# Performance work log

Hardware: AMD Instinct MI355X
Metric: run time of the kernel (lower is better)

The kernel has to match this reference:

```python
import jax, jax.numpy as jnp
import numpy as np

EPS = 1e-6
TEMPERATURE = 0.75
SINKHORN_ITERS = 7
BUCKETS = 128


def setup_inputs() -> dict:
    key = jax.random.key(0)
    k1, k2, k3, k4, k5 = jax.random.split(key, 5)
    b, h, t, dh = 2, 8, 8192, 128
    q = jax.random.normal(k1, (b, h, t, dh), dtype=jnp.float32)
    k = jax.random.normal(k2, (b, h, t, dh), dtype=jnp.float32)
    v = jax.random.normal(k3, (b, h, t, dh), dtype=jnp.float32)
    # SimpleSortNet linear: (1, heads, 2*dim_head, buckets)
    W_sort = jax.random.normal(k4, (1, h, 2 * dh, BUCKETS), dtype=jnp.float32)
    # uniform noise used to build gumbel samples (torch samples internally)
    u_gumbel = jax.random.uniform(k5, (b * h, BUCKETS, BUCKETS), dtype=jnp.float32)
    return {"q": q, "k": k, "v": v, "W_sort": W_sort, "u_gumbel": u_gumbel}


def _gumbel_sinkhorn(R, u):
    # R >= 0 (post-relu). r = (log(R+eps) + gumbel) / temperature
    g = -jnp.log(-jnp.log(u + EPS) + EPS)
    r = (jnp.log(R + EPS) + g) / TEMPERATURE
    for _ in range(SINKHORN_ITERS):
        r = r - jax.nn.logsumexp(r, axis=2, keepdims=True)
        r = r - jax.nn.logsumexp(r, axis=1, keepdims=True)
    return jnp.exp(r)


def reference(q, k, v, W_sort, u_gumbel):
    b, h, t, dh = q.shape
    dim = h * dh  # full model dim, used for the softmax scale (matches torch)
    bh = b * h
    buckets = W_sort.shape[-1]
    bsz = t // buckets

    qm = q.reshape(bh, t, dh)
    km = k.reshape(bh, t, dh)
    vm = v.reshape(bh, t, dh)

    b_q = qm.reshape(bh, buckets, bsz, dh)
    b_k = km.reshape(bh, buckets, bsz, dh)
    b_v = vm.reshape(bh, buckets, bsz, dh)

    # SimpleSortNet: per-bucket sums of q and k -> linear -> relu
    x = jnp.concatenate([b_q.sum(axis=2), b_k.sum(axis=2)], axis=-1)  # (bh, buckets, 2*dh)
    W = jnp.broadcast_to(W_sort, (b, h, 2 * dh, buckets)).reshape(bh, 2 * dh, buckets)
    R = jax.nn.relu(jnp.einsum('bue,bek->buk', x, W))  # (bh, buckets, buckets)

    R = _gumbel_sinkhorn(R, u_gumbel)

    # zero_all_but_top along dim=2 with k=1 (keep argmax entry per row)
    idx = jnp.argmax(R, axis=2, keepdims=True)  # (bh, buckets, 1)
    mask = jnp.arange(buckets)[None, None, :] == idx
    R = jnp.where(mask, R, 0.0)

    # reorder buckets: butd = sum_v R[buv] * b_k[bvtd]
    b_k_r = jnp.einsum('buv,bvtd->butd', R, b_k)
    b_v_r = jnp.einsum('buv,bvtd->butd', R, b_v)

    b_k_cat = jnp.concatenate([b_k_r, b_k], axis=2)  # (bh, buckets, 2*bsz, dh)
    b_v_cat = jnp.concatenate([b_v_r, b_v], axis=2)

    dots = jnp.einsum('buie,buje->buij', b_q, b_k_cat) * (dim ** -0.5)
    attn = jax.nn.softmax(dots, axis=-1)
    out = jnp.einsum('buij,buje->buie', attn, b_v_cat)  # (bh, buckets, bsz, dh)

    return out.reshape(b, h, t, dh)
```

## Files before the change

kernel.cpp:

```cpp
#include <hip/hip_runtime.h>
#include <hip/hip_bf16.h>

#define T_SEQ   8192
#define DH      128
#define NBH     16
#define NBUCK   128
#define BSZ     64
#define EPSF    1e-6f

#define SWZ(r) (((((r) & 7) ^ (((r) >> 3) & 7))) << 3)

typedef __attribute__((ext_vector_type(8))) __bf16 bf16x8;
typedef __attribute__((ext_vector_type(4))) float  f32x4;

static __device__ __forceinline__ unsigned short f2bf(float f) {
  __bf16 h = (__bf16)f;
  return __builtin_bit_cast(unsigned short, h);
}

__global__ __launch_bounds__(256) void k_bsum(
    const float* __restrict__ q, const float* __restrict__ k,
    float* __restrict__ x) {
  const int u = blockIdx.x, bh = blockIdx.y, which = blockIdx.z;
  const int t = threadIdx.x;
  const int c4g = t & 31;
  const int r0  = (t >> 5) << 3;
  const float* src = which ? k : q;
  const float* p = src + ((size_t)bh * T_SEQ + (size_t)u * BSZ + r0) * DH + c4g * 4;
  float4 acc = {0.f, 0.f, 0.f, 0.f};
  #pragma unroll
  for (int r = 0; r < 8; r++) {
    float4 vv = *(const float4*)(p + (size_t)r * DH);
    acc.x += vv.x; acc.y += vv.y; acc.z += vv.z; acc.w += vv.w;
  }
  __shared__ float4 xr[8][32];
  xr[t >> 5][c4g] = acc;
  __syncthreads();
  if (t < 32) {
    float4 s4 = xr[0][t];
    #pragma unroll
    for (int j = 1; j < 8; j++) {
      float4 o = xr[j][t];
      s4.x += o.x; s4.y += o.y; s4.z += o.z; s4.w += o.w;
    }
    *(float4*)(x + ((size_t)bh * NBUCK + u) * 256 + which * 128 + t * 4) = s4;
  }
}

__global__ __launch_bounds__(128) void k_sortgemm(
    const float* __restrict__ x, const float* __restrict__ W,
    const float* __restrict__ ug, float* __restrict__ rbuf) {
  const int u0 = blockIdx.x * 4, bh = blockIdx.y;
  const int v = threadIdx.x;
  __shared__ float xs[4][256];
  for (int i = v; i < 1024; i += 128)
    xs[i >> 8][i & 255] = x[((size_t)bh * NBUCK + u0 + (i >> 8)) * 256 + (i & 255)];
  __syncthreads();
  const float* Wp = W + (size_t)(bh & 7) * 256 * NBUCK + v;
  float acc0 = 0.f, acc1 = 0.f, acc2 = 0.f, acc3 = 0.f;
  #pragma unroll 16
  for (int e = 0; e < 256; e++) {
    float we = Wp[(size_t)e * NBUCK];
    acc0 += xs[0][e] * we;
    acc1 += xs[1][e] * we;
    acc2 += xs[2][e] * we;
    acc3 += xs[3][e] * we;
  }
  float accs[4] = {acc0, acc1, acc2, acc3};
  #pragma unroll
  for (int j = 0; j < 4; j++) {
    float R = fmaxf(accs[j], 0.f) + EPSF;
    float gu = ug[((size_t)bh * NBUCK + u0 + j) * NBUCK + v] + EPSF;
    float g = -logf(-logf(gu) + EPSF);
    rbuf[((size_t)bh * NBUCK + u0 + j) * NBUCK + v] = (logf(R) + g) * (1.f / 0.75f);
  }
}

__global__ __launch_bounds__(1024) void k_sinkhorn(
    const float* __restrict__ rbuf, int* __restrict__ idxb, float* __restrict__ sb) {
  const int bh = blockIdx.x;
  const int t  = threadIdx.x;
  const int g  = t >> 3;
  const int s  = t & 7;
  __shared__ float rl[128 * 129];
  __shared__ float ca[128], ra[128];

  const float* rb = rbuf + (size_t)bh * (NBUCK * NBUCK);
  for (int i = t; i < NBUCK * NBUCK; i += 1024)
    rl[(i >> 7) * 129 + (i & 127)] = rb[i];
  if (t < 128) ca[t] = 0.f;
  __syncthreads();

  for (int iter = 0; iter < 7; iter++) {
    {
      float vals[16];
      float m = -1e30f;
      #pragma unroll
      for (int i = 0; i < 16; i++) {
        int vv = s * 16 + i;
        vals[i] = rl[g * 129 + vv] + ca[vv];
        m = fmaxf(m, vals[i]);
      }
      m = fmaxf(m, __shfl_xor(m, 1));
      m = fmaxf(m, __shfl_xor(m, 2));
      m = fmaxf(m, __shfl_xor(m, 4));
      float ss = 0.f;
      #pragma unroll
      for (int i = 0; i < 16; i++) ss += __expf(vals[i] - m);
      ss += __shfl_xor(ss, 1);
      ss += __shfl_xor(ss, 2);
      ss += __shfl_xor(ss, 4);
      if (s == 0) ra[g] = -(m + logf(ss));
    }
    __syncthreads();
    {
      float vals[16];
      float m = -1e30f;
      #pragma unroll
      for (int i = 0; i < 16; i++) {
        int uu = s * 16 + i;
        vals[i] = rl[uu * 129 + g] + ra[uu];
        m = fmaxf(m, vals[i]);
      }
      m = fmaxf(m, __shfl_xor(m, 1));
      m = fmaxf(m, __shfl_xor(m, 2));
      m = fmaxf(m, __shfl_xor(m, 4));
      float ss = 0.f;
      #pragma unroll
      for (int i = 0; i < 16; i++) ss += __expf(vals[i] - m);
      ss += __shfl_xor(ss, 1);
      ss += __shfl_xor(ss, 2);
      ss += __shfl_xor(ss, 4);
      if (s == 0) ca[g] = -(m + logf(ss));
    }
    __syncthreads();
  }

  {
    float best = -1e30f; int bi = 0;
    #pragma unroll
    for (int i = 0; i < 16; i++) {
      int vv = s * 16 + i;
      float val = rl[g * 129 + vv] + ca[vv];
      if (val > best) { best = val; bi = vv; }
    }
    #pragma unroll
    for (int d = 1; d < 8; d <<= 1) {
      float ob = __shfl_xor(best, d);
      int   oi = __shfl_xor(bi, d);
      if (ob > best || (ob == best && oi < bi)) { best = ob; bi = oi; }
    }
    if (s == 0) {
      idxb[bh * NBUCK + g] = bi;
      sb[bh * NBUCK + g]   = expf(rl[g * 129 + bi] + ra[g] + ca[bi]);
    }
  }
}

__global__ __launch_bounds__(256) void k_attn(
    const float* __restrict__ q, const float* __restrict__ k, const float* __restrict__ v,
    const int* __restrict__ idxb, const float* __restrict__ sb, float* __restrict__ out) {
  const int u  = blockIdx.x;
  const int bh = blockIdx.y;
  const int t  = threadIdx.x;
  const int lane = t & 63;
  const int w  = t >> 6;
  const int l15 = lane & 15;
  const int lgp = lane >> 4;

  __shared__ uint4 smem4[2048];
  unsigned short* sm = (unsigned short*)smem4;
  #define VOFF 8192

  const int   vidx = idxb[bh * NBUCK + u];
  const float sval = sb[bh * NBUCK + u];
  const size_t hb = (size_t)bh * (T_SEQ * DH);
  const float* qg = q + hb;
  const float* kg = k + hb;
  const float* vg = v + hb;

  #pragma unroll
  for (int it = 0; it < 16; it++) {
    int i = it * 256 + t;
    int row = i >> 5;
    int c4 = (i & 31) << 2;
    int grow = (row < 64) ? (vidx * BSZ + row) : (u * BSZ + (row - 64));
    float4 val = *(const float4*)(kg + (size_t)grow * DH + c4);
    ushort4 hh;
    hh.x = f2bf(val.x); hh.y = f2bf(val.y); hh.z = f2bf(val.z); hh.w = f2bf(val.w);
    *(ushort4*)(sm + (((row * 128 + c4) ^ SWZ(row)))) = hh;
  }

  bf16x8 aQ[4];
  {
    int qrow = u * BSZ + w * 16 + l15;
    const float* qp = qg + (size_t)qrow * DH + lgp * 8;
    #pragma unroll
    for (int kk = 0; kk < 4; kk++) {
      float4 v0 = *(const float4*)(qp + kk * 32);
      float4 v1 = *(const float4*)(qp + kk * 32 + 4);
      bf16x8 f;
      f[0] = (__bf16)v0.x; f[1] = (__bf16)v0.y; f[2] = (__bf16)v0.z; f[3] = (__bf16)v0.w;
      f[4] = (__bf16)v1.x; f[5] = (__bf16)v1.y; f[6] = (__bf16)v1.z; f[7] = (__bf16)v1.w;
      aQ[kk] = f;
    }
  }

  float4 vpre1[8], vpre2[8];
  #pragma unroll
  for (int it = 0; it < 8; it++) {
    int i = it * 256 + t;
    int d0 = (i & 31) << 2;
    int j  = i >> 5;
    vpre1[it] = *(const float4*)(vg + (size_t)(vidx * BSZ + j) * DH + d0);
    vpre2[it] = *(const float4*)(vg + (size_t)(u    * BSZ + j) * DH + d0);
  }
  __syncthreads();

  f32x4 accS[8];
  #pragma unroll
  for (int n = 0; n < 8; n++) {
    f32x4 acc = {0.f, 0.f, 0.f, 0.f};
    #pragma unroll
    for (int kk = 0; kk < 4; kk++) {
      int row = n * 16 + l15;
      int c0 = lgp * 8 + kk * 32;
      bf16x8 bK = *(const bf16x8*)(sm + ((row * 128 + c0) ^ SWZ(row)));
      acc = __builtin_amdgcn_mfma_f32_16x16x32_bf16(aQ[kk], bK, acc, 0, 0, 0);
    }
    accS[n] = acc;
  }

  float pval[8][4];
  float lsum[4];
  #pragma unroll
  for (int r = 0; r < 4; r++) {
    float mm = -1e30f;
    #pragma unroll
    for (int n = 0; n < 8; n++) {
      float lg2 = accS[n][r] * 0.03125f * (n < 4 ? sval : 1.0f);
      pval[n][r] = lg2;
      mm = fmaxf(mm, lg2);
    }
    mm = fmaxf(mm, __shfl_xor(mm, 1));
    mm = fmaxf(mm, __shfl_xor(mm, 2));
    mm = fmaxf(mm, __shfl_xor(mm, 4));
    mm = fmaxf(mm, __shfl_xor(mm, 8));
    float ss = 0.f;
    #pragma unroll
    for (int n = 0; n < 8; n++) {
      float p = __expf(pval[n][r] - mm);
      ss += p;
      pval[n][r] = p * (n < 4 ? sval : 1.0f);
    }
    ss += __shfl_xor(ss, 1);
    ss += __shfl_xor(ss, 2);
    ss += __shfl_xor(ss, 4);
    ss += __shfl_xor(ss, 8);
    lsum[r] = ss;
  }

  __syncthreads();

  #pragma unroll
  for (int n = 0; n < 8; n++) {
    #pragma unroll
    for (int r = 0; r < 4; r++) {
      int prow = w * 16 + lgp * 4 + r;
      int pcol = n * 16 + l15;
      sm[(prow * 128 + pcol) ^ SWZ(prow)] = f2bf(pval[n][r]);
    }
  }
  #pragma unroll
  for (int it = 0; it < 8; it++) {
    int i = it * 256 + t;
    int d0 = (i & 31) << 2;
    int j  = i >> 5;
    float4 val = vpre1[it];
    sm[VOFF + (((d0 + 0) * 64 + j) ^ SWZ(d0 + 0))] = f2bf(val.x);
    sm[VOFF + (((d0 + 1) * 64 + j) ^ SWZ(d0 + 1))] = f2bf(val.y);
    sm[VOFF + (((d0 + 2) * 64 + j) ^ SWZ(d0 + 2))] = f2bf(val.z);
    sm[VOFF + (((d0 + 3) * 64 + j) ^ SWZ(d0 + 3))] = f2bf(val.w);
  }
  __syncthreads();

  bf16x8 aP[4];
  #pragma unroll
  for (int kk = 0; kk < 4; kk++) {
    int prow = w * 16 + l15;
    int c0 = lgp * 8 + kk * 32;
    aP[kk] = *(const bf16x8*)(sm + ((prow * 128 + c0) ^ SWZ(prow)));
  }

  f32x4 accO[8];
  #pragma unroll
  for (int n = 0; n < 8; n++) {
    f32x4 acc = {0.f, 0.f, 0.f, 0.f};
    #pragma unroll
    for (int kk = 0; kk < 2; kk++) {
      int d = n * 16 + l15;
      int jj0 = lgp * 8 + kk * 32;
      bf16x8 bV = *(const bf16x8*)(sm + VOFF + ((d * 64 + jj0) ^ SWZ(d)));
      acc = __builtin_amdgcn_mfma_f32_16x16x32_bf16(aP[kk], bV, acc, 0, 0, 0);
    }
    accO[n] = acc;
  }
  __syncthreads();

  #pragma unroll
  for (int it = 0; it < 8; it++) {
    int i = it * 256 + t;
    int d0 = (i & 31) << 2;
    int j  = i >> 5;
    float4 val = vpre2[it];
    sm[VOFF + (((d0 + 0) * 64 + j) ^ SWZ(d0 + 0))] = f2bf(val.x);
    sm[VOFF + (((d0 + 1) * 64 + j) ^ SWZ(d0 + 1))] = f2bf(val.y);
    sm[VOFF + (((d0 + 2) * 64 + j) ^ SWZ(d0 + 2))] = f2bf(val.z);
    sm[VOFF + (((d0 + 3) * 64 + j) ^ SWZ(d0 + 3))] = f2bf(val.w);
  }
  __syncthreads();

  float invl[4];
  #pragma unroll
  for (int r = 0; r < 4; r++) invl[r] = 1.0f / lsum[r];

  #pragma unroll
  for (int n = 0; n < 8; n++) {
    f32x4 acc = accO[n];
    #pragma unroll
    for (int kk = 2; kk < 4; kk++) {
      int d = n * 16 + l15;
      int jj0 = lgp * 8 + (kk - 2) * 32;
      bf16x8 bV = *(const bf16x8*)(sm + VOFF + ((d * 64 + jj0) ^ SWZ(d)));
      acc = __builtin_amdgcn_mfma_f32_16x16x32_bf16(aP[kk], bV, acc, 0, 0, 0);
    }
    #pragma unroll
    for (int r = 0; r < 4; r++) {
      int i2 = w * 16 + lgp * 4 + r;
      int d = n * 16 + l15;
      out[((size_t)bh * T_SEQ + (size_t)u * BSZ + i2) * DH + d] = acc[r] * invl[r];
    }
  }
}

extern "C" void kernel_launch(void* const* d_in, const int* in_sizes, int n_in,
                              void* d_out, int out_size, void* d_ws, size_t ws_size,
                              hipStream_t stream) {
  (void)in_sizes; (void)n_in; (void)out_size; (void)ws_size;
  const float* q  = (const float*)d_in[0];
  const float* k  = (const float*)d_in[1];
  const float* v  = (const float*)d_in[2];
  const float* W  = (const float*)d_in[3];
  const float* ug = (const float*)d_in[4];
  float* out = (float*)d_out;

  float* xbuf = (float*)d_ws;
  float* rbuf = xbuf + (size_t)NBH * NBUCK * 256;
  int*   idxb = (int*)(rbuf + (size_t)NBH * NBUCK * NBUCK);
  float* sb   = (float*)(idxb + NBH * NBUCK);

  k_bsum    <<<dim3(NBUCK, NBH, 2), 256, 0, stream>>>(q, k, xbuf);
  k_sortgemm<<<dim3(32, NBH),       128, 0, stream>>>(xbuf, W, ug, rbuf);
  k_sinkhorn<<<NBH,                1024, 0, stream>>>(rbuf, idxb, sb);
  k_attn    <<<dim3(NBUCK, NBH),    256, 0, stream>>>(q, k, v, idxb, sb, out);
}
```

Measured before the change: 121.1 us.

## Cache Sinkhorn rows/cols in registers and reorder attention loads with setprio

The Sinkhorn kernel now runs with 512 threads, four per row, and keeps each thread's row and column slice in registers. This removes the repeated shared-memory reads in every iteration, and the exp sums are split across four partial accumulators. The attention kernel issues all K and Q global loads before converting them, and delays the second V prefetch until after the first V tile is written, to lower register pressure. It also adds launch bounds for occupancy and raises wave priority around the MFMA loops. The risks are register spills from the larger per-thread arrays and less latency hiding for the late V load.

```diff
diff --git a/kernel.cpp b/kernel.cpp
--- a/kernel.cpp
+++ b/kernel.cpp
@@ -76,88 +76,113 @@
   }
 }
 
-__global__ __launch_bounds__(1024) void k_sinkhorn(
+__global__ __launch_bounds__(512, 1) void k_sinkhorn(
     const float* __restrict__ rbuf, int* __restrict__ idxb, float* __restrict__ sb) {
   const int bh = blockIdx.x;
   const int t  = threadIdx.x;
-  const int g  = t >> 3;
-  const int s  = t & 7;
+  const int own = t >> 2;
+  const int qq  = t & 3;
   __shared__ float rl[128 * 129];
   __shared__ float ca[128], ra[128];
 
   const float* rb = rbuf + (size_t)bh * (NBUCK * NBUCK);
-  for (int i = t; i < NBUCK * NBUCK; i += 1024)
+  for (int i = t; i < NBUCK * NBUCK; i += 512)
     rl[(i >> 7) * 129 + (i & 127)] = rb[i];
   if (t < 128) ca[t] = 0.f;
   __syncthreads();
 
+  float rowv[32], colv[32];
+  #pragma unroll
+  for (int i4 = 0; i4 < 8; i4++) {
+    float4 vv = *(const float4*)(&rl[own * 129 + qq * 32 + i4 * 4]);
+    rowv[i4 * 4 + 0] = vv.x; rowv[i4 * 4 + 1] = vv.y;
+    rowv[i4 * 4 + 2] = vv.z; rowv[i4 * 4 + 3] = vv.w;
+  }
+  #pragma unroll
+  for (int i = 0; i < 32; i++) colv[i] = rl[(qq * 32 + i) * 129 + own];
+
   for (int iter = 0; iter < 7; iter++) {
     {
-      float vals[16];
+      float vals[32];
       float m = -1e30f;
       #pragma unroll
-      for (int i = 0; i < 16; i++) {
-        int vv = s * 16 + i;
-        vals[i] = rl[g * 129 + vv] + ca[vv];
-        m = fmaxf(m, vals[i]);
+      for (int i4 = 0; i4 < 8; i4++) {
+        float4 cc = *(const float4*)(&ca[qq * 32 + i4 * 4]);
+        vals[i4 * 4 + 0] = rowv[i4 * 4 + 0] + cc.x;
+        vals[i4 * 4 + 1] = rowv[i4 * 4 + 1] + cc.y;
+        vals[i4 * 4 + 2] = rowv[i4 * 4 + 2] + cc.z;
+        vals[i4 * 4 + 3] = rowv[i4 * 4 + 3] + cc.w;
       }
+      #pragma unroll
+      for (int i = 0; i < 32; i++) m = fmaxf(m, vals[i]);
       m = fmaxf(m, __shfl_xor(m, 1));
       m = fmaxf(m, __shfl_xor(m, 2));
-      m = fmaxf(m, __shfl_xor(m, 4));
-      float ss = 0.f;
-      #pragma unroll
-      for (int i = 0; i < 16; i++) ss += __expf(vals[i] - m);
+      float s0 = 0.f, s1 = 0.f, s2 = 0.f, s3 = 0.f;
+      #pragma unroll
+      for (int i = 0; i < 8; i++) {
+        s0 += __expf(vals[i * 4 + 0] - m);
+        s1 += __expf(vals[i * 4 + 1] - m);
+        s2 += __expf(vals[i * 4 + 2] - m);
+        s3 += __expf(vals[i * 4 + 3] - m);
+      }
+      float ss = (s0 + s1) + (s2 + s3);
       ss += __shfl_xor(ss, 1);
       ss += __shfl_xor(ss, 2);
-      ss += __shfl_xor(ss, 4);
-      if (s == 0) ra[g] = -(m + logf(ss));
+      if (qq == 0) ra[own] = -(m + logf(ss));
     }
     __syncthreads();
     {
-      float vals[16];
+      float vals[32];
       float m = -1e30f;
       #pragma unroll
-      for (int i = 0; i < 16; i++) {
-        int uu = s * 16 + i;
-        vals[i] = rl[uu * 129 + g] + ra[uu];
-        m = fmaxf(m, vals[i]);
+      for (int i4 = 0; i4 < 8; i4++) {
+        float4 rr = *(const float4*)(&ra[qq * 32 + i4 * 4]);
+        vals[i4 * 4 + 0] = colv[i4 * 4 + 0] + rr.x;
+        vals[i4 * 4 + 1] = colv[i4 * 4 + 1] + rr.y;
+        vals[i4 * 4 + 2] = colv[i4 * 4 + 2] + rr.z;
+        vals[i4 * 4 + 3] = colv[i4 * 4 + 3] + rr.w;
       }
+      #pragma unroll
+      for (int i = 0; i < 32; i++) m = fmaxf(m, vals[i]);
       m = fmaxf(m, __shfl_xor(m, 1));
       m = fmaxf(m, __shfl_xor(m, 2));
-      m = fmaxf(m, __shfl_xor(m, 4));
-      float ss = 0.f;
-      #pragma unroll
-      for (int i = 0; i < 16; i++) ss += __expf(vals[i] - m);
+      float s0 = 0.f, s1 = 0.f, s2 = 0.f, s3 = 0.f;
+      #pragma unroll
+      for (int i = 0; i < 8; i++) {
+        s0 += __expf(vals[i * 4 + 0] - m);
+        s1 += __expf(vals[i * 4 + 1] - m);
+        s2 += __expf(vals[i * 4 + 2] - m);
+        s3 += __expf(vals[i * 4 + 3] - m);
+      }
+      float ss = (s0 + s1) + (s2 + s3);
       ss += __shfl_xor(ss, 1);
       ss += __shfl_xor(ss, 2);
-      ss += __shfl_xor(ss, 4);
-      if (s == 0) ca[g] = -(m + logf(ss));
+      if (qq == 0) ca[own] = -(m + logf(ss));
     }
     __syncthreads();
   }
 
   {
-    float best = -1e30f; int bi = 0;
-    #pragma unroll
-    for (int i = 0; i < 16; i++) {
-      int vv = s * 16 + i;
-      float val = rl[g * 129 + vv] + ca[vv];
-      if (val > best) { best = val; bi = vv; }
-    }
-    #pragma unroll
-    for (int d = 1; d < 8; d <<= 1) {
+    float best = -1e30f; int bi = qq * 32;
+    #pragma unroll
+    for (int i = 0; i < 32; i++) {
+      float val = rowv[i] + ca[qq * 32 + i];
+      if (val > best) { best = val; bi = qq * 32 + i; }
+    }
+    #pragma unroll
+    for (int d = 1; d < 4; d <<= 1) {
       float ob = __shfl_xor(best, d);
       int   oi = __shfl_xor(bi, d);
       if (ob > best || (ob == best && oi < bi)) { best = ob; bi = oi; }
     }
-    if (s == 0) {
-      idxb[bh * NBUCK + g] = bi;
-      sb[bh * NBUCK + g]   = expf(rl[g * 129 + bi] + ra[g] + ca[bi]);
-    }
-  }
-}
-
-__global__ __launch_bounds__(256) void k_attn(
+    if (qq == 0) {
+      idxb[bh * NBUCK + own] = bi;
+      sb[bh * NBUCK + own]   = expf(rl[own * 129 + bi] + ra[own] + ca[bi]);
+    }
+  }
+}
+
+__global__ __launch_bounds__(256, 5) void k_attn(
     const float* __restrict__ q, const float* __restrict__ k, const float* __restrict__ v,
     const int* __restrict__ idxb, const float* __restrict__ sb, float* __restrict__ out) {
   const int u  = blockIdx.x;
@@ -179,45 +204,58 @@
   const float* kg = k + hb;
   const float* vg = v + hb;
 
+  float4 kr[16];
   #pragma unroll
   for (int it = 0; it < 16; it++) {
     int i = it * 256 + t;
     int row = i >> 5;
     int c4 = (i & 31) << 2;
     int grow = (row < 64) ? (vidx * BSZ + row) : (u * BSZ + (row - 64));
-    float4 val = *(const float4*)(kg + (size_t)grow * DH + c4);
+    kr[it] = *(const float4*)(kg + (size_t)grow * DH + c4);
+  }
+  float4 qf[8];
+  {
+    int qrow = u * BSZ + w * 16 + l15;
+    const float* qp = qg + (size_t)qrow * DH + lgp * 8;
+    #pragma unroll
+    for (int kk = 0; kk < 4; kk++) {
+      qf[kk * 2 + 0] = *(const float4*)(qp + kk * 32);
+      qf[kk * 2 + 1] = *(const float4*)(qp + kk * 32 + 4);
+    }
+  }
+  #pragma unroll
+  for (int it = 0; it < 16; it++) {
+    int i = it * 256 + t;
+    int row = i >> 5;
+    int c4 = (i & 31) << 2;
+    float4 val = kr[it];
     ushort4 hh;
     hh.x = f2bf(val.x); hh.y = f2bf(val.y); hh.z = f2bf(val.z); hh.w = f2bf(val.w);
     *(ushort4*)(sm + (((row * 128 + c4) ^ SWZ(row)))) = hh;
   }
-
-  bf16x8 aQ[4];
-  {
-    int qrow = u * BSZ + w * 16 + l15;
-    const float* qp = qg + (size_t)qrow * DH + lgp * 8;
-    #pragma unroll
-    for (int kk = 0; kk < 4; kk++) {
-      float4 v0 = *(const float4*)(qp + kk * 32);
-      float4 v1 = *(const float4*)(qp + kk * 32 + 4);
-      bf16x8 f;
-      f[0] = (__bf16)v0.x; f[1] = (__bf16)v0.y; f[2] = (__bf16)v0.z; f[3] = (__bf16)v0.w;
-      f[4] = (__bf16)v1.x; f[5] = (__bf16)v1.y; f[6] = (__bf16)v1.z; f[7] = (__bf16)v1.w;
-      aQ[kk] = f;
-    }
-  }
-
-  float4 vpre1[8], vpre2[8];
+  float4 vpre1[8];
   #pragma unroll
   for (int it = 0; it < 8; it++) {
     int i = it * 256 + t;
     int d0 = (i & 31) << 2;
     int j  = i >> 5;
     vpre1[it] = *(const float4*)(vg + (size_t)(vidx * BSZ + j) * DH + d0);
-    vpre2[it] = *(const float4*)(vg + (size_t)(u    * BSZ + j) * DH + d0);
-  }
-  __syncthreads();
+  }
+  __syncthreads();
+
+  bf16x8 aQ[4];
+  #pragma unroll
+  for (int kk = 0; kk < 4; kk++) {
+    float4 v0 = qf[kk * 2 + 0];
+    float4 v1 = qf[kk * 2 + 1];
+    bf16x8 f;
+    f[0] = (__bf16)v0.x; f[1] = (__bf16)v0.y; f[2] = (__bf16)v0.z; f[3] = (__bf16)v0.w;
+    f[4] = (__bf16)v1.x; f[5] = (__bf16)v1.y; f[6] = (__bf16)v1.z; f[7] = (__bf16)v1.w;
+    aQ[kk] = f;
+  }
 
   f32x4 accS[8];
+  __builtin_amdgcn_s_setprio(1);
   #pragma unroll
   for (int n = 0; n < 8; n++) {
     f32x4 acc = {0.f, 0.f, 0.f, 0.f};
@@ -230,6 +268,7 @@
     }
     accS[n] = acc;
   }
+  __builtin_amdgcn_s_setprio(0);
 
   float pval[8][4];
   float lsum[4];
@@ -282,6 +321,14 @@
     sm[VOFF + (((d0 + 2) * 64 + j) ^ SWZ(d0 + 2))] = f2bf(val.z);
     sm[VOFF + (((d0 + 3) * 64 + j) ^ SWZ(d0 + 3))] = f2bf(val.w);
   }
+  float4 vpre2[8];
+  #pragma unroll
+  for (int it = 0; it < 8; it++) {
+    int i = it * 256 + t;
+    int d0 = (i & 31) << 2;
+    int j  = i >> 5;
+    vpre2[it] = *(const float4*)(vg + (size_t)(u * BSZ + j) * DH + d0);
+  }
   __syncthreads();
 
   bf16x8 aP[4];
@@ -293,6 +340,7 @@
   }
 
   f32x4 accO[8];
+  __builtin_amdgcn_s_setprio(1);
   #pragma unroll
   for (int n = 0; n < 8; n++) {
     f32x4 acc = {0.f, 0.f, 0.f, 0.f};
@@ -305,6 +353,7 @@
     }
     accO[n] = acc;
   }
+  __builtin_amdgcn_s_setprio(0);
   __syncthreads();
 
   #pragma unroll
@@ -324,6 +373,7 @@
   #pragma unroll
   for (int r = 0; r < 4; r++) invl[r] = 1.0f / lsum[r];
 
+  __builtin_amdgcn_s_setprio(1);
   #pragma unroll
   for (int n = 0; n < 8; n++) {
     f32x4 acc = accO[n];
@@ -341,6 +391,7 @@
       out[((size_t)bh * T_SEQ + (size_t)u * BSZ + i2) * DH + d] = acc[r] * invl[r];
     }
   }
+  __builtin_amdgcn_s_setprio(0);
 }
 
 extern "C" void kernel_launch(void* const* d_in, const int* in_sizes, int n_in,
@@ -361,6 +412,6 @@
 
   k_bsum    <<<dim3(NBUCK, NBH, 2), 256, 0, stream>>>(q, k, xbuf);
   k_sortgemm<<<dim3(32, NBH),       128, 0, stream>>>(xbuf, W, ug, rbuf);
-  k_sinkhorn<<<NBH,                1024, 0, stream>>>(rbuf, idxb, sb);
+  k_sinkhorn<<<NBH,                 512, 0, stream>>>(rbuf, idxb, sb);
   k_attn    <<<dim3(NBUCK, NBH),    256, 0, stream>>>(q, k, v, idxb, sb, out);
 }
```

New measurement: 174.0 us. +43.6%, slower.
